# Kernel optimization log

Measured on AMD Instinct MI355X. Metric: run time of the kernel, lower is better.

## Reference

```python
import jax, jax.numpy as jnp
import numpy as np

N = 100000       # num vertices
M = 200000       # num hyperedges
NNZ = 1600000    # num incidences
NFEAT = 128
NHID = 64        # nhid * nhead = 8 * 8
NCLASS = 40
NLAYER = 8
ALPHA = 0.1
LAMDA = 0.5


def setup_inputs() -> dict:
    key = jax.random.key(0)
    ks = jax.random.split(key, 10)
    x = jax.random.normal(ks[0], (N, NFEAT), jnp.float32)
    vertex = jax.random.randint(ks[1], (NNZ,), 0, N)
    edges = jax.random.randint(ks[2], (NNZ,), 0, M)
    degE = jax.random.uniform(ks[3], (M, 1), jnp.float32)
    degV = jax.random.uniform(ks[4], (N, 1), jnp.float32)
    s0 = 1.0 / np.sqrt(NFEAT)
    s1 = 1.0 / np.sqrt(NHID)
    W0 = jax.random.uniform(ks[5], (NFEAT, NHID), jnp.float32, -s0, s0)
    b0 = jnp.zeros((NHID,), jnp.float32)
    Ws = jax.random.uniform(ks[6], (NLAYER, NHID, NHID), jnp.float32, -s1, s1)
    Wout = jax.random.uniform(ks[7], (NHID, NCLASS), jnp.float32, -s1, s1)
    bout = jnp.zeros((NCLASS,), jnp.float32)
    return {"x": x, "vertex": vertex, "edges": edges, "degE": degE, "degV": degV,
            "W0": W0, "b0": b0, "Ws": Ws, "Wout": Wout, "bout": bout}


def reference(x, vertex, edges, degE, degV, W0, b0, Ws, Wout, bout):
    # scatter-mean denominator: #incidences per hyperedge
    counts = jax.ops.segment_sum(jnp.ones((NNZ,), x.dtype), edges, num_segments=M)
    inv_counts = jnp.where(counts > 0, 1.0 / counts, 0.0)[:, None]  # [M,1]

    h = jax.nn.relu(x @ W0 + b0)   # input linear (dropout is identity in eval)
    h0 = h                         # initial residual
    for i in range(NLAYER):
        beta = float(np.log(LAMDA / (i + 1) + 1.0))
        # vertex -> edge gather + scatter-mean, scale by degE
        Xe = jax.ops.segment_sum(h[vertex], edges, num_segments=M) * inv_counts * degE  # [M,H]
        # edge -> vertex gather + scatter-sum, scale by degV
        Xv = jax.ops.segment_sum(Xe[edges], vertex, num_segments=N) * degV              # [N,H]
        # L2 row-normalize (norm is detached in the original)
        rn = jax.lax.stop_gradient(jnp.linalg.norm(Xv, axis=1, keepdims=True))
        Xv = Xv * jnp.where(rn > 0, 1.0 / rn, 0.0)
        # GCNII initial-residual + identity mixing
        Xi = (1.0 - ALPHA) * Xv + ALPHA * h0
        h = jax.nn.relu((1.0 - beta) * Xi + beta * (Xi @ Ws[i]))
    return h @ Wout + bout
```

## Files before the change

kernel.cpp:

```cpp
#include <hip/hip_runtime.h>
#include <math.h>

#define N_V    100000
#define N_E    200000
#define NNZ_C  1600000
#define NFEAT  128
#define NHID   64
#define NCLASS 40
#define NLAYER 8
#define ALPHA  0.1f

#define NWIN   8
#define WE     (N_E / NWIN)
#define WV     (N_V / NWIN)

#define MAXDE  48
#define MAXDV  64

typedef _Float16 f16;
typedef _Float16 f16x8 __attribute__((ext_vector_type(8)));

__global__ __launch_bounds__(256) void k_place(const int* __restrict__ vertex,
                                               const int* __restrict__ edges,
                                               int* __restrict__ cntE,
                                               int* __restrict__ cntV,
                                               int* __restrict__ scrE,
                                               int* __restrict__ scrV) {
    const int win  = blockIdx.x & (NWIN - 1);
    const int blk  = blockIdx.x >> 3;
    const int nblk = gridDim.x >> 3;
    const int eLo = win * WE, eHi = eLo + WE;
    const int vLo = win * WV, vHi = vLo + WV;
    for (int z = blk * blockDim.x + threadIdx.x; z < NNZ_C; z += nblk * blockDim.x) {
        int v = __builtin_nontemporal_load(&vertex[z]);
        int e = __builtin_nontemporal_load(&edges[z]);
        if (e >= eLo && e < eHi) {
            int p = atomicAdd(&cntE[e], 1);
            if (p < MAXDE) scrE[e * MAXDE + p] = v;
        }
        if (v >= vLo && v < vHi) {
            int p = atomicAdd(&cntV[v], 1);
            if (p < MAXDV) scrV[v * MAXDV + p] = e;
        }
    }
}

__global__ __launch_bounds__(256) void k_factor(const int* __restrict__ cntE,
                                                const float* __restrict__ degE,
                                                float* __restrict__ factorE) {
    int e = blockIdx.x * blockDim.x + threadIdx.x;
    if (e < N_E) {
        int c = cntE[e];
        factorE[e] = (c > 0) ? degE[e] / (float)c : 0.0f;
    }
}

__global__ __launch_bounds__(256) void k_lin(const float* __restrict__ x,
                                             const float* __restrict__ W0,
                                             const float* __restrict__ b0,
                                             f16* __restrict__ h,
                                             f16* __restrict__ h0) {
    __shared__ float sW[NFEAT * NHID];
    __shared__ float sb[NHID];
    for (int i = threadIdx.x; i < NFEAT * NHID; i += blockDim.x) sW[i] = W0[i];
    if (threadIdx.x < NHID) sb[threadIdx.x] = b0[threadIdx.x];
    __syncthreads();
    const int lane = threadIdx.x & 63;
    const int t    = lane & 7;
    const int pair = blockIdx.x * 32 + (threadIdx.x >> 3);
    if (pair >= N_V / 2) return;
    const int r0 = 2 * pair, r1 = r0 + 1;
    const float4* __restrict__ x4 = (const float4*)x;
    float xr0[16], xr1[16];
    #pragma unroll
    for (int i = 0; i < 4; ++i) {
        float4 q0 = x4[(size_t)r0 * 32 + t * 4 + i];
        float4 q1 = x4[(size_t)r1 * 32 + t * 4 + i];
        xr0[4 * i + 0] = q0.x; xr0[4 * i + 1] = q0.y;
        xr0[4 * i + 2] = q0.z; xr0[4 * i + 3] = q0.w;
        xr1[4 * i + 0] = q1.x; xr1[4 * i + 1] = q1.y;
        xr1[4 * i + 2] = q1.z; xr1[4 * i + 3] = q1.w;
    }
    float a0[8], a1[8];
    #pragma unroll
    for (int j = 0; j < 8; ++j) { a0[j] = sb[8 * t + j]; a1[j] = a0[j]; }
    const int sgbase = lane & 56;
    #pragma unroll
    for (int k = 0; k < NFEAT; ++k) {
        float xk0 = __shfl(xr0[k & 15], sgbase | (k >> 4), 64);
        float xk1 = __shfl(xr1[k & 15], sgbase | (k >> 4), 64);
        const float4 wa = *(const float4*)&sW[k * NHID + 8 * t];
        const float4 wb = *(const float4*)&sW[k * NHID + 8 * t + 4];
        a0[0] = fmaf(xk0, wa.x, a0[0]);  a1[0] = fmaf(xk1, wa.x, a1[0]);
        a0[1] = fmaf(xk0, wa.y, a0[1]);  a1[1] = fmaf(xk1, wa.y, a1[1]);
        a0[2] = fmaf(xk0, wa.z, a0[2]);  a1[2] = fmaf(xk1, wa.z, a1[2]);
        a0[3] = fmaf(xk0, wa.w, a0[3]);  a1[3] = fmaf(xk1, wa.w, a1[3]);
        a0[4] = fmaf(xk0, wb.x, a0[4]);  a1[4] = fmaf(xk1, wb.x, a1[4]);
        a0[5] = fmaf(xk0, wb.y, a0[5]);  a1[5] = fmaf(xk1, wb.y, a1[5]);
        a0[6] = fmaf(xk0, wb.z, a0[6]);  a1[6] = fmaf(xk1, wb.z, a1[6]);
        a0[7] = fmaf(xk0, wb.w, a0[7]);  a1[7] = fmaf(xk1, wb.w, a1[7]);
    }
    f16x8 o0, o1;
    #pragma unroll
    for (int j = 0; j < 8; ++j) {
        o0[j] = (f16)fmaxf(a0[j], 0.0f);
        o1[j] = (f16)fmaxf(a1[j], 0.0f);
    }
    ((f16x8*)h )[(size_t)r0 * 8 + t] = o0;
    ((f16x8*)h )[(size_t)r1 * 8 + t] = o1;
    ((f16x8*)h0)[(size_t)r0 * 8 + t] = o0;
    ((f16x8*)h0)[(size_t)r1 * 8 + t] = o1;
}

__global__ __launch_bounds__(256) void k_edge_gather(const int* __restrict__ cntE,
                                                     const int* __restrict__ scrE,
                                                     const float* __restrict__ factorE,
                                                     const f16* __restrict__ h,
                                                     f16* __restrict__ Xe) {
    const int lane = threadIdx.x & 63;
    const int sg = lane >> 3, t = lane & 7;
    const int e = (blockIdx.x * 4 + (threadIdx.x >> 6)) * 8 + sg;
    if (e >= N_E) return;
    const f16x8* __restrict__ hv = (const f16x8*)h;
    const int cnt = min(cntE[e], MAXDE);
    const int base = e * MAXDE;
    const float fac = factorE[e];
    float acc[8] = {0.f, 0.f, 0.f, 0.f, 0.f, 0.f, 0.f, 0.f};
    for (int w = 0; w < cnt; w += 4) {
        int4 q = *(const int4*)&scrE[base + w];
        int i0 = q.x;
        int i1 = (w + 1 < cnt) ? q.y : q.x;
        int i2 = (w + 2 < cnt) ? q.z : q.x;
        int i3 = (w + 3 < cnt) ? q.w : q.x;
        float m1 = (w + 1 < cnt) ? 1.f : 0.f;
        float m2 = (w + 2 < cnt) ? 1.f : 0.f;
        float m3 = (w + 3 < cnt) ? 1.f : 0.f;
        f16x8 v0 = hv[(size_t)i0 * 8 + t];
        f16x8 v1 = hv[(size_t)i1 * 8 + t];
        f16x8 v2 = hv[(size_t)i2 * 8 + t];
        f16x8 v3 = hv[(size_t)i3 * 8 + t];
        #pragma unroll
        for (int j = 0; j < 8; ++j) {
            acc[j] += (float)v0[j];
            acc[j] = fmaf(m1, (float)v1[j], acc[j]);
            acc[j] = fmaf(m2, (float)v2[j], acc[j]);
            acc[j] = fmaf(m3, (float)v3[j], acc[j]);
        }
    }
    f16x8 o;
    #pragma unroll
    for (int j = 0; j < 8; ++j) o[j] = (f16)(acc[j] * fac);
    ((f16x8*)Xe)[(size_t)e * 8 + t] = o;
}

__global__ __launch_bounds__(256) void k_vertex_update(const int* __restrict__ cntV,
                                                       const int* __restrict__ scrV,
                                                       const f16* __restrict__ Xe,
                                                       const float* __restrict__ degV,
                                                       const f16* __restrict__ h0,
                                                       const float* __restrict__ Wi,
                                                       float beta,
                                                       f16* __restrict__ h) {
    __shared__ float sW[NHID * NHID];
    for (int i = threadIdx.x; i < NHID * NHID; i += blockDim.x) sW[i] = Wi[i];
    __syncthreads();
    const int lane = threadIdx.x & 63;
    const int sg = lane >> 3, t = lane & 7;
    const int n = (blockIdx.x * 4 + (threadIdx.x >> 6)) * 8 + sg;
    if (n >= N_V) return;
    const f16x8* __restrict__ xe = (const f16x8*)Xe;
    const int cnt = min(cntV[n], MAXDV);
    const int base = n * MAXDV;
    const float dv = degV[n];
    const f16x8 h0v = ((const f16x8*)h0)[(size_t)n * 8 + t];
    float acc[8] = {0.f, 0.f, 0.f, 0.f, 0.f, 0.f, 0.f, 0.f};
    for (int w = 0; w < cnt; w += 8) {
        int4 qa = *(const int4*)&scrV[base + w];
        int4 qb = *(const int4*)&scrV[base + w + 4];
        int   idx[8];
        float msk[8];
        idx[0] = qa.x;                       msk[0] = 1.f;
        idx[1] = (w + 1 < cnt) ? qa.y : qa.x; msk[1] = (w + 1 < cnt) ? 1.f : 0.f;
        idx[2] = (w + 2 < cnt) ? qa.z : qa.x; msk[2] = (w + 2 < cnt) ? 1.f : 0.f;
        idx[3] = (w + 3 < cnt) ? qa.w : qa.x; msk[3] = (w + 3 < cnt) ? 1.f : 0.f;
        idx[4] = (w + 4 < cnt) ? qb.x : qa.x; msk[4] = (w + 4 < cnt) ? 1.f : 0.f;
        idx[5] = (w + 5 < cnt) ? qb.y : qa.x; msk[5] = (w + 5 < cnt) ? 1.f : 0.f;
        idx[6] = (w + 6 < cnt) ? qb.z : qa.x; msk[6] = (w + 6 < cnt) ? 1.f : 0.f;
        idx[7] = (w + 7 < cnt) ? qb.w : qa.x; msk[7] = (w + 7 < cnt) ? 1.f : 0.f;
        f16x8 v[8];
        #pragma unroll
        for (int r = 0; r < 8; ++r) v[r] = xe[(size_t)idx[r] * 8 + t];
        #pragma unroll
        for (int j = 0; j < 8; ++j) {
            #pragma unroll
            for (int r = 0; r < 8; ++r)
                acc[j] = fmaf(msk[r], (float)v[r][j], acc[j]);
        }
    }
    float xv[8], ss = 0.f;
    #pragma unroll
    for (int j = 0; j < 8; ++j) { xv[j] = acc[j] * dv; ss = fmaf(xv[j], xv[j], ss); }
    #pragma unroll
    for (int off = 1; off <= 4; off <<= 1)
        ss += __shfl_xor(ss, off, 64);
    float rn  = sqrtf(ss);
    float inv = (rn > 0.0f) ? 1.0f / rn : 0.0f;
    float xi[8];
    #pragma unroll
    for (int j = 0; j < 8; ++j)
        xi[j] = (1.0f - ALPHA) * (xv[j] * inv) + ALPHA * (float)h0v[j];
    float y[8] = {0.f, 0.f, 0.f, 0.f, 0.f, 0.f, 0.f, 0.f};
    #pragma unroll
    for (int k = 0; k < NHID; ++k) {
        float xk = __shfl(xi[k & 7], 8 * sg + (k >> 3), 64);
        const float4 wa = *(const float4*)&sW[k * NHID + 8 * t];
        const float4 wb = *(const float4*)&sW[k * NHID + 8 * t + 4];
        y[0] = fmaf(xk, wa.x, y[0]);
        y[1] = fmaf(xk, wa.y, y[1]);
        y[2] = fmaf(xk, wa.z, y[2]);
        y[3] = fmaf(xk, wa.w, y[3]);
        y[4] = fmaf(xk, wb.x, y[4]);
        y[5] = fmaf(xk, wb.y, y[5]);
        y[6] = fmaf(xk, wb.z, y[6]);
        y[7] = fmaf(xk, wb.w, y[7]);
    }
    f16x8 o;
    #pragma unroll
    for (int j = 0; j < 8; ++j) {
        float v = fmaf(beta, y[j] - xi[j], xi[j]);
        o[j] = (f16)fmaxf(v, 0.0f);
    }
    ((f16x8*)h)[(size_t)n * 8 + t] = o;
}

__global__ __launch_bounds__(256) void k_out(const f16* __restrict__ h,
                                             const float* __restrict__ Wout,
                                             const float* __restrict__ bout,
                                             float* __restrict__ out) {
    __shared__ float sW[NHID * NCLASS];
    __shared__ float sb[NCLASS];
    for (int i = threadIdx.x; i < NHID * NCLASS; i += blockDim.x) sW[i] = Wout[i];
    if (threadIdx.x < NCLASS) sb[threadIdx.x] = bout[threadIdx.x];
    __syncthreads();
    const int lane   = threadIdx.x & 63;
    const int t      = lane & 7;
    const int sgbase = lane & 56;
    const int pair   = blockIdx.x * 32 + (threadIdx.x >> 3);
    if (pair >= N_V / 2) return;
    const int r0 = 2 * pair, r1 = r0 + 1;
    const f16x8 hv0 = ((const f16x8*)h)[(size_t)r0 * 8 + t];
    const f16x8 hv1 = ((const f16x8*)h)[(size_t)r1 * 8 + t];
    float h0r[8], h1r[8];
    #pragma unroll
    for (int j = 0; j < 8; ++j) { h0r[j] = (float)hv0[j]; h1r[j] = (float)hv1[j]; }
    float y0[5], y1[5];
    #pragma unroll
    for (int i = 0; i < 5; ++i) { y0[i] = sb[t + 8 * i]; y1[i] = y0[i]; }
    #pragma unroll
    for (int k = 0; k < NHID; ++k) {
        float hk0 = __shfl(h0r[k & 7], sgbase | (k >> 3), 64);
        float hk1 = __shfl(h1r[k & 7], sgbase | (k >> 3), 64);
        const float* wr = &sW[k * NCLASS];
        #pragma unroll
        for (int i = 0; i < 5; ++i) {
            float w = wr[t + 8 * i];
            y0[i] = fmaf(hk0, w, y0[i]);
            y1[i] = fmaf(hk1, w, y1[i]);
        }
    }
    #pragma unroll
    for (int i = 0; i < 5; ++i) {
        out[(size_t)r0 * NCLASS + t + 8 * i] = y0[i];
        out[(size_t)r1 * NCLASS + t + 8 * i] = y1[i];
    }
}

extern "C" void kernel_launch(void* const* d_in, const int* in_sizes, int n_in,
                              void* d_out, int out_size, void* d_ws, size_t ws_size,
                              hipStream_t stream) {
    const float* x      = (const float*)d_in[0];
    const int*   vertex = (const int*)  d_in[1];
    const int*   edges  = (const int*)  d_in[2];
    const float* degE   = (const float*)d_in[3];
    const float* degV   = (const float*)d_in[4];
    const float* W0     = (const float*)d_in[5];
    const float* b0     = (const float*)d_in[6];
    const float* Ws     = (const float*)d_in[7];
    const float* Wout   = (const float*)d_in[8];
    const float* bout   = (const float*)d_in[9];
    float* out = (float*)d_out;

    char* p = (char*)d_ws;
    auto carve = [&](size_t bytes) { char* r = p; p += (bytes + 255) & ~(size_t)255; return r; };
    f16*   h0      = (f16*)  carve((size_t)N_V * NHID * sizeof(f16));
    f16*   hA      = (f16*)  carve((size_t)N_V * NHID * sizeof(f16));
    f16*   Xe      = (f16*)  carve((size_t)N_E * NHID * sizeof(f16));
    float* factorE = (float*)carve((size_t)N_E * sizeof(float));
    int*   cntE    = (int*)  carve((size_t)N_E * sizeof(int));
    int*   cntV    = (int*)  carve((size_t)N_V * sizeof(int));
    int*   scrE    = (int*)  carve((size_t)N_E * MAXDE * sizeof(int));
    int*   scrV    = (int*)  carve((size_t)N_V * MAXDV * sizeof(int));

    hipMemsetAsync(cntE, 0, (size_t)(N_E + N_V) * sizeof(int), stream);
    k_place <<<NWIN * 256, 256, 0, stream>>>(vertex, edges, cntE, cntV, scrE, scrV);
    k_factor<<<(N_E + 255) / 256, 256, 0, stream>>>(cntE, degE, factorE);

    k_lin<<<(N_V / 2 + 31) / 32, 256, 0, stream>>>(x, W0, b0, hA, h0);

    for (int i = 0; i < NLAYER; ++i) {
        float beta = (float)log(0.5 / (double)(i + 1) + 1.0);
        k_edge_gather  <<<(N_E + 31) / 32, 256, 0, stream>>>(cntE, scrE, factorE, hA, Xe);
        k_vertex_update<<<(N_V + 31) / 32, 256, 0, stream>>>(cntV, scrV, Xe, degV, h0,
                                                             Ws + (size_t)i * NHID * NHID,
                                                             beta, hA);
    }
    k_out<<<(N_V / 2 + 31) / 32, 256, 0, stream>>>(hA, Wout, bout, out);
}
```

Baseline: 927.1 us.

## Split h and Xe into four column chunks and map chunks to XCDs in edge gather

Stores h and Xe in a chunked layout: four column slices of 16 features, each contiguous across all rows. The edge-gather kernel gives each XCD-pinned block one feature chunk, so each XCD's L2 holds a quarter-size working set of h. The aim is fewer L2 misses on the random gathers. In exchange each gather is a 4-byte load instead of 16-byte, and there are four times more index reads. The separate factor kernel is folded into the gather.

```diff
diff --git a/kernel.cpp b/kernel.cpp
--- a/kernel.cpp
+++ b/kernel.cpp
@@ -19,6 +19,9 @@
 
 typedef _Float16 f16;
 typedef _Float16 f16x8 __attribute__((ext_vector_type(8)));
+typedef _Float16 f16x2 __attribute__((ext_vector_type(2)));
+typedef int      v4i   __attribute__((ext_vector_type(4)));
+
 
 __global__ __launch_bounds__(256) void k_place(const int* __restrict__ vertex,
                                                const int* __restrict__ edges,
@@ -45,16 +48,6 @@
     }
 }
 
-__global__ __launch_bounds__(256) void k_factor(const int* __restrict__ cntE,
-                                                const float* __restrict__ degE,
-                                                float* __restrict__ factorE) {
-    int e = blockIdx.x * blockDim.x + threadIdx.x;
-    if (e < N_E) {
-        int c = cntE[e];
-        factorE[e] = (c > 0) ? degE[e] / (float)c : 0.0f;
-    }
-}
-
 __global__ __launch_bounds__(256) void k_lin(const float* __restrict__ x,
                                              const float* __restrict__ W0,
                                              const float* __restrict__ b0,
@@ -106,51 +99,56 @@
         o0[j] = (f16)fmaxf(a0[j], 0.0f);
         o1[j] = (f16)fmaxf(a1[j], 0.0f);
     }
-    ((f16x8*)h )[(size_t)r0 * 8 + t] = o0;
-    ((f16x8*)h )[(size_t)r1 * 8 + t] = o1;
+    const size_t hci = (size_t)(t >> 1) * (N_V * 2) + (t & 1);
+    ((f16x8*)h )[hci + (size_t)r0 * 2] = o0;
+    ((f16x8*)h )[hci + (size_t)r1 * 2] = o1;
     ((f16x8*)h0)[(size_t)r0 * 8 + t] = o0;
     ((f16x8*)h0)[(size_t)r1 * 8 + t] = o1;
 }
 
-__global__ __launch_bounds__(256) void k_edge_gather(const int* __restrict__ cntE,
-                                                     const int* __restrict__ scrE,
-                                                     const float* __restrict__ factorE,
-                                                     const f16* __restrict__ h,
-                                                     f16* __restrict__ Xe) {
-    const int lane = threadIdx.x & 63;
-    const int sg = lane >> 3, t = lane & 7;
-    const int e = (blockIdx.x * 4 + (threadIdx.x >> 6)) * 8 + sg;
-    if (e >= N_E) return;
-    const f16x8* __restrict__ hv = (const f16x8*)h;
-    const int cnt = min(cntE[e], MAXDE);
-    const int base = e * MAXDE;
-    const float fac = factorE[e];
-    float acc[8] = {0.f, 0.f, 0.f, 0.f, 0.f, 0.f, 0.f, 0.f};
+__global__ __launch_bounds__(256) void k_egather(const int* __restrict__ cntE,
+                                                 const int* __restrict__ scrE,
+                                                 const float* __restrict__ degE,
+                                                 const f16* __restrict__ h,
+                                                 f16* __restrict__ Xe) {
+    const int xcd = blockIdx.x & 7;
+    const int c   = xcd & 3;
+    const int j   = ((blockIdx.x >> 3) << 1) | (xcd >> 2);
+    const int sg  = threadIdx.x >> 3, t = threadIdx.x & 7;
+    const int e   = j * 32 + sg;
+    const f16x2* __restrict__ hc = (const f16x2*)(h + (size_t)c * (N_V * 16));
+    f16x2* __restrict__ xc = (f16x2*)(Xe + (size_t)c * (N_E * 16));
+    const int cnt = min(__builtin_nontemporal_load(&cntE[e]), MAXDE);
+    const float de = __builtin_nontemporal_load(&degE[e]);
+    const float fac = (cnt > 0) ? de / (float)cnt : 0.0f;
+    const v4i* __restrict__ sr = (const v4i*)(scrE + (size_t)e * MAXDE);
+    float a0 = 0.f, a1 = 0.f;
     for (int w = 0; w < cnt; w += 4) {
-        int4 q = *(const int4*)&scrE[base + w];
-        int i0 = q.x;
-        int i1 = (w + 1 < cnt) ? q.y : q.x;
-        int i2 = (w + 2 < cnt) ? q.z : q.x;
-        int i3 = (w + 3 < cnt) ? q.w : q.x;
+        v4i q = __builtin_nontemporal_load(&sr[w >> 2]);
+        int i0 = q[0];
+        int i1 = (w + 1 < cnt) ? q[1] : q[0];
+        int i2 = (w + 2 < cnt) ? q[2] : q[0];
+        int i3 = (w + 3 < cnt) ? q[3] : q[0];
         float m1 = (w + 1 < cnt) ? 1.f : 0.f;
         float m2 = (w + 2 < cnt) ? 1.f : 0.f;
         float m3 = (w + 3 < cnt) ? 1.f : 0.f;
-        f16x8 v0 = hv[(size_t)i0 * 8 + t];
-        f16x8 v1 = hv[(size_t)i1 * 8 + t];
-        f16x8 v2 = hv[(size_t)i2 * 8 + t];
-        f16x8 v3 = hv[(size_t)i3 * 8 + t];
-        #pragma unroll
-        for (int j = 0; j < 8; ++j) {
-            acc[j] += (float)v0[j];
-            acc[j] = fmaf(m1, (float)v1[j], acc[j]);
-            acc[j] = fmaf(m2, (float)v2[j], acc[j]);
-            acc[j] = fmaf(m3, (float)v3[j], acc[j]);
-        }
-    }
-    f16x8 o;
-    #pragma unroll
-    for (int j = 0; j < 8; ++j) o[j] = (f16)(acc[j] * fac);
-    ((f16x8*)Xe)[(size_t)e * 8 + t] = o;
+        f16x2 v0 = hc[(size_t)i0 * 8 + t];
+        f16x2 v1 = hc[(size_t)i1 * 8 + t];
+        f16x2 v2 = hc[(size_t)i2 * 8 + t];
+        f16x2 v3 = hc[(size_t)i3 * 8 + t];
+        a0 += (float)v0[0];
+        a0 = fmaf(m1, (float)v1[0], a0);
+        a0 = fmaf(m2, (float)v2[0], a0);
+        a0 = fmaf(m3, (float)v3[0], a0);
+        a1 += (float)v0[1];
+        a1 = fmaf(m1, (float)v1[1], a1);
+        a1 = fmaf(m2, (float)v2[1], a1);
+        a1 = fmaf(m3, (float)v3[1], a1);
+    }
+    f16x2 o;
+    o[0] = (f16)(a0 * fac);
+    o[1] = (f16)(a1 * fac);
+    xc[(size_t)e * 8 + t] = o;
 }
 
 __global__ __launch_bounds__(256) void k_vertex_update(const int* __restrict__ cntV,
@@ -168,7 +166,8 @@
     const int sg = lane >> 3, t = lane & 7;
     const int n = (blockIdx.x * 4 + (threadIdx.x >> 6)) * 8 + sg;
     if (n >= N_V) return;
-    const f16x8* __restrict__ xe = (const f16x8*)Xe;
+    const f16x8* __restrict__ xe8 = (const f16x8*)Xe;
+    const size_t xcb = (size_t)(t >> 1) * (N_E * 2) + (t & 1);
     const int cnt = min(cntV[n], MAXDV);
     const int base = n * MAXDV;
     const float dv = degV[n];
@@ -189,7 +188,7 @@
         idx[7] = (w + 7 < cnt) ? qb.w : qa.x; msk[7] = (w + 7 < cnt) ? 1.f : 0.f;
         f16x8 v[8];
         #pragma unroll
-        for (int r = 0; r < 8; ++r) v[r] = xe[(size_t)idx[r] * 8 + t];
+        for (int r = 0; r < 8; ++r) v[r] = xe8[xcb + (size_t)idx[r] * 2];
         #pragma unroll
         for (int j = 0; j < 8; ++j) {
             #pragma unroll
@@ -230,7 +229,7 @@
         float v = fmaf(beta, y[j] - xi[j], xi[j]);
         o[j] = (f16)fmaxf(v, 0.0f);
     }
-    ((f16x8*)h)[(size_t)n * 8 + t] = o;
+    ((f16x8*)h)[(size_t)(t >> 1) * (N_V * 2) + (size_t)n * 2 + (t & 1)] = o;
 }
 
 __global__ __launch_bounds__(256) void k_out(const f16* __restrict__ h,
@@ -248,8 +247,9 @@
     const int pair   = blockIdx.x * 32 + (threadIdx.x >> 3);
     if (pair >= N_V / 2) return;
     const int r0 = 2 * pair, r1 = r0 + 1;
-    const f16x8 hv0 = ((const f16x8*)h)[(size_t)r0 * 8 + t];
-    const f16x8 hv1 = ((const f16x8*)h)[(size_t)r1 * 8 + t];
+    const size_t hci = (size_t)(t >> 1) * (N_V * 2) + (t & 1);
+    const f16x8 hv0 = ((const f16x8*)h)[hci + (size_t)r0 * 2];
+    const f16x8 hv1 = ((const f16x8*)h)[hci + (size_t)r1 * 2];
     float h0r[8], h1r[8];
     #pragma unroll
     for (int j = 0; j < 8; ++j) { h0r[j] = (float)hv0[j]; h1r[j] = (float)hv1[j]; }
@@ -295,21 +295,19 @@
     f16*   h0      = (f16*)  carve((size_t)N_V * NHID * sizeof(f16));
     f16*   hA      = (f16*)  carve((size_t)N_V * NHID * sizeof(f16));
     f16*   Xe      = (f16*)  carve((size_t)N_E * NHID * sizeof(f16));
-    float* factorE = (float*)carve((size_t)N_E * sizeof(float));
     int*   cntE    = (int*)  carve((size_t)N_E * sizeof(int));
     int*   cntV    = (int*)  carve((size_t)N_V * sizeof(int));
     int*   scrE    = (int*)  carve((size_t)N_E * MAXDE * sizeof(int));
     int*   scrV    = (int*)  carve((size_t)N_V * MAXDV * sizeof(int));
 
     hipMemsetAsync(cntE, 0, (size_t)(N_E + N_V) * sizeof(int), stream);
-    k_place <<<NWIN * 256, 256, 0, stream>>>(vertex, edges, cntE, cntV, scrE, scrV);
-    k_factor<<<(N_E + 255) / 256, 256, 0, stream>>>(cntE, degE, factorE);
+    k_place<<<NWIN * 256, 256, 0, stream>>>(vertex, edges, cntE, cntV, scrE, scrV);
 
     k_lin<<<(N_V / 2 + 31) / 32, 256, 0, stream>>>(x, W0, b0, hA, h0);
 
     for (int i = 0; i < NLAYER; ++i) {
         float beta = (float)log(0.5 / (double)(i + 1) + 1.0);
-        k_edge_gather  <<<(N_E + 31) / 32, 256, 0, stream>>>(cntE, scrE, factorE, hA, Xe);
+        k_egather<<<8 * 3125, 256, 0, stream>>>(cntE, scrE, degE, hA, Xe);
         k_vertex_update<<<(N_V + 31) / 32, 256, 0, stream>>>(cntV, scrV, Xe, degV, h0,
                                                              Ws + (size_t)i * NHID * NHID,
                                                              beta, hA);
```

Result: slower. 1.823 ms (median of 2 runs) (+96.6%).
